# Kernel optimization log

Hardware: AMD Instinct MI355X
Metric: run time of the kernel (lower is better)

## Reference

```python
import jax, jax.numpy as jnp
import numpy as np

B, T, F, H = 64, 512, 128, 512

def _rnn(x_seq, h0, Wih, Whh, bih, bhh):
    # PyTorch vanilla RNN: h_t = tanh(x_t @ Wih^T + bih + h_{t-1} @ Whh^T + bhh)
    def step(h, x_t):
        h = jnp.tanh(x_t @ Wih.T + bih + h @ Whh.T + bhh)
        return h, h
    _, ys = jax.lax.scan(step, h0, jnp.swapaxes(x_seq, 0, 1))  # scan over time
    return jnp.swapaxes(ys, 0, 1)  # [B, T, H]

def _decode(z, Wih, Whh, bih, bhh):
    # decoder input at step t = concat(prev_output, z_t); 1-layer RNN so prev_output == h_{t-1}
    def step(h, z_t):
        u = jnp.concatenate([h, z_t], axis=-1)  # [B, 2H]
        h_new = jnp.tanh(u @ Wih.T + bih + h @ Whh.T + bhh)
        return h_new, h_new
    h0 = jnp.zeros((z.shape[0], Whh.shape[0]), z.dtype)
    _, ys = jax.lax.scan(step, h0, jnp.swapaxes(z, 0, 1))
    return jnp.swapaxes(ys, 0, 1)  # [B, T, H]

def setup_inputs() -> dict:
    key = jax.random.key(0)
    ks = jax.random.split(key, 16)
    s = 0.02
    p = {
        'x':   jax.random.normal(ks[0], (B, T, F), jnp.float32),
        'eps': jax.random.normal(ks[1], (B, T, H), jnp.float32),
        'Wih_en': jax.random.normal(ks[2], (H, F)) * s,
        'Whh_en': jax.random.normal(ks[3], (H, H)) * s,
        'bih_en': jax.random.normal(ks[4], (H,)) * s,
        'bhh_en': jax.random.normal(ks[5], (H,)) * s,
        'W_mu':  jax.random.normal(ks[6], (H, H)) * s,
        'b_mu':  jax.random.normal(ks[7], (H,)) * s,
        'W_lv':  jax.random.normal(ks[8], (H, H)) * s,
        'b_lv':  jax.random.normal(ks[9], (H,)) * s,
        'Wih_de': jax.random.normal(ks[10], (H, 2 * H)) * s,
        'Whh_de': jax.random.normal(ks[11], (H, H)) * s,
        'bih_de': jax.random.normal(ks[12], (H,)) * s,
        'bhh_de': jax.random.normal(ks[13], (H,)) * s,
        'W_mux': jax.random.normal(ks[14], (F, H)) * s,
        'b_mux': jnp.zeros((F,)),
        'W_lvx': jax.random.normal(ks[15], (F, H)) * s,
        'b_lvx': jnp.zeros((F,)),
    }
    return p

def reference(x, eps, Wih_en, Whh_en, bih_en, bhh_en, W_mu, b_mu, W_lv, b_lv,
              Wih_de, Whh_de, bih_de, bhh_de, W_mux, b_mux, W_lvx, b_lvx):
    h0 = jnp.zeros((x.shape[0], Whh_en.shape[0]), x.dtype)
    y = _rnn(x, h0, Wih_en, Whh_en, bih_en, bhh_en)                 # [B,T,H]
    mu_post = y @ W_mu.T + b_mu
    logsigma2_post = y @ W_lv.T + b_lv
    z = eps * jnp.exp(logsigma2_post / 2) + mu_post                 # reparameterize
    outputs = _decode(z, Wih_de, Whh_de, bih_de, bhh_de)            # [B,T,H]
    mu_xhat = outputs @ W_mux.T + b_mux
    logsigma2_xhat = outputs @ W_lvx.T + b_lvx
    return (mu_post, logsigma2_post, mu_xhat, logsigma2_xhat)
```

## Files before the change

kernel.cpp:

```cpp
#include <hip/hip_runtime.h>

typedef _Float16 h2_t __attribute__((ext_vector_type(2)));
typedef _Float16 h4_t __attribute__((ext_vector_type(4)));
typedef _Float16 h8_t __attribute__((ext_vector_type(8)));
typedef float    f4_t __attribute__((ext_vector_type(4)));

#define B_  64
#define T_  512
#define F_  128
#define H_  512

static __device__ __forceinline__ int d4(int acc, unsigned a, unsigned b) {
#if __has_builtin(__builtin_amdgcn_sdot4)
    return __builtin_amdgcn_sdot4((int)a, (int)b, acc, false);
#else
    #pragma unroll
    for (int i = 0; i < 4; ++i)
        acc += (int)(signed char)((a >> (8 * i)) & 0xff) *
               (int)(signed char)((b >> (8 * i)) & 0xff);
    return acc;
#endif
}
static __device__ __forceinline__ int dot16i8(int acc, uint4 w, uint4 h) {
    acc = d4(acc, w.x, h.x);
    acc = d4(acc, w.y, h.y);
    acc = d4(acc, w.z, h.z);
    acc = d4(acc, w.w, h.w);
    return acc;
}

static __device__ __forceinline__ int pair_sum(int x) {
#if __has_builtin(__builtin_amdgcn_mov_dpp)
    return x + __builtin_amdgcn_mov_dpp(x, 0xB1, 0xF, 0xF, true);
#else
    return x + __shfl_xor(x, 1);
#endif
}

__global__ void k_cast_f16(const float* __restrict__ src, _Float16* __restrict__ dst, int n) {
    int i = blockIdx.x * blockDim.x + threadIdx.x;
    if (i < n) dst[i] = (_Float16)src[i];
}

__global__ void k_prep_z(const float* __restrict__ Wih_de, _Float16* __restrict__ Wz) {
    int i = blockIdx.x * blockDim.x + threadIdx.x;
    int cc = i >> 9, kk = i & 511;
    Wz[i] = (_Float16)Wih_de[cc * 1024 + 512 + kk];
}

__global__ void k_prep_bias(const float* __restrict__ a, const float* __restrict__ b,
                            float* __restrict__ o) {
    int i = threadIdx.x;
    o[i] = a[i] + b[i];
}

__global__ void k_cat2(const float* __restrict__ a, const float* __restrict__ b,
                       float* __restrict__ o, int n) {
    int i = blockIdx.x * blockDim.x + threadIdx.x;
    if (i < 2 * n) o[i] = (i < n) ? a[i] : b[i - n];
}

__global__ void k_quant(const float* __restrict__ A, int sA,
                        const float* __restrict__ Bo, int sB,
                        signed char* __restrict__ q, float* __restrict__ fac) {
    __shared__ float red[128];
    const int c = blockIdx.x, t = threadIdx.x;
    f4_t v = *(const f4_t*)(A + (size_t)c * sA + t * 4);
    if (Bo) {
        f4_t vb = *(const f4_t*)(Bo + (size_t)c * sB + t * 4);
        v = v + vb;
    }
    float m = fmaxf(fmaxf(fabsf(v[0]), fabsf(v[1])), fmaxf(fabsf(v[2]), fabsf(v[3])));
    red[t] = m;
    __syncthreads();
    for (int o = 64; o; o >>= 1) {
        if (t < o) red[t] = fmaxf(red[t], red[t + o]);
        __syncthreads();
    }
    float mx = red[0];
    float inv = mx > 0.f ? 127.f / mx : 0.f;
    unsigned r = 0;
    #pragma unroll
    for (int i = 0; i < 4; ++i) {
        int qi = (int)rintf(fminf(fmaxf(v[i] * inv, -127.f), 127.f));
        r |= ((unsigned)(unsigned char)(signed char)qi) << (8 * i);
    }
    *(unsigned*)(q + (size_t)c * 512 + t * 4) = r;
    if (t == 0) fac[c] = mx > 0.f ? mx / 127.f : 0.f;
}

#define BM 128
#define BN 128
#define BK 32
#define LDT 40

__global__ __launch_bounds__(256) void k_gemm(
    const _Float16* __restrict__ A, const _Float16* __restrict__ Bt,
    const float* __restrict__ bias,
    float* __restrict__ Cf, float* __restrict__ Cf2, _Float16* __restrict__ Ch,
    int M, int N, int nsplit, int K) {
    __shared__ _Float16 Al[BM * LDT];
    __shared__ _Float16 Bl[BN * LDT];
    const int tid = threadIdx.x;
    const int bm = blockIdx.x * BM, bn = blockIdx.y * BN;
    const int wid = tid >> 6, lane = tid & 63;
    const int wm = (wid >> 1) * 64, wn = (wid & 1) * 64;
    const int l15 = lane & 15, l4 = lane >> 4;

    f4_t acc[4][4];
    #pragma unroll
    for (int i = 0; i < 4; ++i)
        #pragma unroll
        for (int j = 0; j < 4; ++j) {
            f4_t zz = {0.f, 0.f, 0.f, 0.f};
            acc[i][j] = zz;
        }

    const int r = tid >> 1, hf = tid & 1;
    const h8_t* gA0 = (const h8_t*)(A + (size_t)(bm + r) * K);
    const h8_t* gB0 = (const h8_t*)(Bt + (size_t)(bn + r) * K);

    for (int k0 = 0; k0 < K; k0 += BK) {
        __syncthreads();
        int kf = (k0 >> 3) + hf * 2;
        h8_t a0 = gA0[kf], a1 = gA0[kf + 1];
        h8_t b0 = gB0[kf], b1 = gB0[kf + 1];
        *(h8_t*)&Al[r * LDT + hf * 16]     = a0;
        *(h8_t*)&Al[r * LDT + hf * 16 + 8] = a1;
        *(h8_t*)&Bl[r * LDT + hf * 16]     = b0;
        *(h8_t*)&Bl[r * LDT + hf * 16 + 8] = b1;
        __syncthreads();
        h8_t af[4], bf[4];
        #pragma unroll
        for (int i = 0; i < 4; ++i) af[i] = *(const h8_t*)&Al[(wm + i * 16 + l15) * LDT + l4 * 8];
        #pragma unroll
        for (int j = 0; j < 4; ++j) bf[j] = *(const h8_t*)&Bl[(wn + j * 16 + l15) * LDT + l4 * 8];
        #pragma unroll
        for (int i = 0; i < 4; ++i)
            #pragma unroll
            for (int j = 0; j < 4; ++j)
                acc[i][j] = __builtin_amdgcn_mfma_f32_16x16x32_f16(af[i], bf[j], acc[i][j], 0, 0, 0);
    }

    const int ns2 = N - nsplit;
    #pragma unroll
    for (int i = 0; i < 4; ++i) {
        int m0 = bm + wm + i * 16 + l4 * 4;
        #pragma unroll
        for (int j = 0; j < 4; ++j) {
            int n0 = bn + wn + j * 16 + l15;
            float bb = bias ? bias[n0] : 0.f;
            #pragma unroll
            for (int rr = 0; rr < 4; ++rr) {
                float v = acc[i][j][rr] + bb;
                if (Cf) {
                    if (n0 < nsplit) Cf[(size_t)(m0 + rr) * nsplit + n0] = v;
                    else             Cf2[(size_t)(m0 + rr) * ns2 + (n0 - nsplit)] = v;
                }
                if (Ch) Ch[(size_t)(m0 + rr) * N + n0] = (_Float16)v;
            }
        }
    }
}

#define HHS 272
__global__ __launch_bounds__(512) void k_rnn(
    const signed char* __restrict__ Wq,
    const float* __restrict__ fac,
    const _Float16* __restrict__ pre,
    _Float16* __restrict__ out) {
    __shared__ __align__(16) signed char h_q[2][2 * HHS];

    const int tid = threadIdx.x;
    const int half = tid & 1;
    const int r0 = tid & ~1;
    const int r1 = tid | 1;
    const int b = blockIdx.x;

    const uint4* q0 = (const uint4*)(Wq + (size_t)r0 * 512 + half * 256);
    const uint4* q1 = (const uint4*)(Wq + (size_t)r1 * 512 + half * 256);
    uint4 wa[16], wb[16];
    #pragma unroll
    for (int j = 0; j < 16; ++j) { wa[j] = q0[j]; wb[j] = q1[j]; }
    if (tid < 34) ((uint4*)&h_q[0][0])[tid] = make_uint4(0u, 0u, 0u, 0u);
    __syncthreads();

    const size_t base = (size_t)b * T_ * H_ + tid;
    float pcur = (float)pre[base];
    const float facr = fac[tid] * (1.f / 127.f);
    const int woff = ((tid >> 8) * HHS) + (tid & 255);

    for (int t = 0; t < T_; ++t) {
        int tn = (t + 1 < T_) ? t + 1 : t;
        _Float16 pnx = pre[base + (size_t)tn * H_];

        int i0 = 0, i1 = 0;
        const uint4* hv = (const uint4*)&h_q[t & 1][half * HHS];
        #pragma unroll
        for (int j = 0; j < 16; ++j) {
            uint4 hh = hv[j];
            i0 = dot16i8(i0, wa[j], hh);
            i1 = dot16i8(i1, wb[j], hh);
        }

        int o0 = pair_sum(i0);
        int o1 = pair_sum(i1);
        int mine = half ? o1 : o0;

        float hn = tanhf((float)mine * facr + pcur);
        out[base + (size_t)t * H_] = (_Float16)hn;
        h_q[(t + 1) & 1][woff] = (signed char)(int)rintf(hn * 127.f);
        __syncthreads();
        pcur = (float)pnx;
    }
}

__global__ void k_z(const float* __restrict__ mu, const float* __restrict__ lv,
                    const float* __restrict__ eps, _Float16* __restrict__ z, int n4) {
    int i = blockIdx.x * blockDim.x + threadIdx.x;
    if (i >= n4) return;
    f4_t m = ((const f4_t*)mu)[i];
    f4_t l = ((const f4_t*)lv)[i];
    f4_t e = ((const f4_t*)eps)[i];
    h4_t r;
    #pragma unroll
    for (int j = 0; j < 4; ++j) r[j] = (_Float16)(e[j] * expf(l[j] * 0.5f) + m[j]);
    ((h4_t*)z)[i] = r;
}

extern "C" void kernel_launch(void* const* d_in, const int* in_sizes, int n_in,
                              void* d_out, int out_size, void* d_ws, size_t ws_size,
                              hipStream_t stream) {
    const float* x      = (const float*)d_in[0];
    const float* eps    = (const float*)d_in[1];
    const float* Wih_en = (const float*)d_in[2];
    const float* Whh_en = (const float*)d_in[3];
    const float* bih_en = (const float*)d_in[4];
    const float* bhh_en = (const float*)d_in[5];
    const float* W_mu   = (const float*)d_in[6];
    const float* b_mu   = (const float*)d_in[7];
    const float* W_lv   = (const float*)d_in[8];
    const float* b_lv   = (const float*)d_in[9];
    const float* Wih_de = (const float*)d_in[10];
    const float* Whh_de = (const float*)d_in[11];
    const float* bih_de = (const float*)d_in[12];
    const float* bhh_de = (const float*)d_in[13];
    const float* W_mux  = (const float*)d_in[14];
    const float* b_mux  = (const float*)d_in[15];
    const float* W_lvx  = (const float*)d_in[16];
    const float* b_lvx  = (const float*)d_in[17];
    float* out = (float*)d_out;

    char* ws = (char*)d_ws;
    _Float16* Wih_en_h = (_Float16*)(ws + 0);
    _Float16* W_mu_h   = (_Float16*)(ws + 655360);
    _Float16* W_lv_h   = (_Float16*)(ws + 1179648);
    _Float16* Wz_h     = (_Float16*)(ws + 1703936);
    _Float16* Wmux_h   = (_Float16*)(ws + 2752512);
    _Float16* Wlvx_h   = (_Float16*)(ws + 2883584);
    float*    benc     = (float*)(ws + 3014656);
    float*    bdec     = (float*)(ws + 3016704);
    signed char* Wq_en = (signed char*)(ws + 3018752);
    signed char* Wq_de = (signed char*)(ws + 3280896);
    float*    fac_en   = (float*)(ws + 3543040);
    float*    fac_de   = (float*)(ws + 3545088);
    float*    bmulv    = (float*)(ws + 3547136);
    float*    bmuxlvx  = (float*)(ws + 3551232);
    _Float16* x_h      = (_Float16*)(ws + 4194304);
    _Float16* pre_h    = (_Float16*)(ws + 12582912);
    _Float16* act_h    = (_Float16*)(ws + 46137344);
    _Float16* z_h      = (_Float16*)(ws + 79691776);

    const int thr = 256;
    k_cast_f16<<<(65536 + thr - 1) / thr, thr, 0, stream>>>(Wih_en, Wih_en_h, 65536);
    k_cast_f16<<<(262144 + thr - 1) / thr, thr, 0, stream>>>(W_mu, W_mu_h, 262144);
    k_cast_f16<<<(262144 + thr - 1) / thr, thr, 0, stream>>>(W_lv, W_lv_h, 262144);
    k_cast_f16<<<(65536 + thr - 1) / thr, thr, 0, stream>>>(W_mux, Wmux_h, 65536);
    k_cast_f16<<<(65536 + thr - 1) / thr, thr, 0, stream>>>(W_lvx, Wlvx_h, 65536);
    k_cast_f16<<<(4194304 + thr - 1) / thr, thr, 0, stream>>>(x, x_h, 4194304);
    k_prep_z<<<262144 / thr, thr, 0, stream>>>(Wih_de, Wz_h);
    k_prep_bias<<<1, 512, 0, stream>>>(bih_en, bhh_en, benc);
    k_prep_bias<<<1, 512, 0, stream>>>(bih_de, bhh_de, bdec);
    k_cat2<<<4, 256, 0, stream>>>(b_mu, b_lv, bmulv, 512);
    k_cat2<<<1, 256, 0, stream>>>(b_mux, b_lvx, bmuxlvx, 128);
    k_quant<<<512, 128, 0, stream>>>(Whh_en, 512, nullptr, 0, Wq_en, fac_en);
    k_quant<<<512, 128, 0, stream>>>(Wih_de, 1024, Whh_de, 512, Wq_de, fac_de);

    dim3 gFull(32768 / BM, 512 / BN);
    dim3 gWide(32768 / BM, 1024 / BN);
    dim3 gNarrow(32768 / BM, 256 / BN);

    k_gemm<<<gFull, 256, 0, stream>>>(x_h, Wih_en_h, benc, nullptr, nullptr, pre_h,
                                      32768, 512, 512, 128);
    k_rnn<<<64, 512, 0, stream>>>(Wq_en, fac_en, pre_h, act_h);
    k_gemm<<<gWide, 256, 0, stream>>>(act_h, W_mu_h, bmulv, out, out + 16777216, nullptr,
                                      32768, 1024, 512, 512);
    k_z<<<4194304 / thr, thr, 0, stream>>>(out, out + 16777216, eps, z_h, 4194304);
    k_gemm<<<gFull, 256, 0, stream>>>(z_h, Wz_h, bdec, nullptr, nullptr, pre_h,
                                      32768, 512, 512, 512);
    k_rnn<<<64, 512, 0, stream>>>(Wq_de, fac_de, pre_h, act_h);
    k_gemm<<<gNarrow, 256, 0, stream>>>(act_h, Wmux_h, bmuxlvx, out + 33554432, out + 37748736,
                                        nullptr, 32768, 256, 128, 512);
}
```

Measured before the change: 1.084 ms.

## Repack int8 recurrent weights coalesced and spill part of them to global reads

Adds a repack kernel that lays out the int8 recurrent weights so that consecutive threads read consecutive uint4 words. The RNN kernel now keeps only 10 of 16 weight chunks per row in registers and streams the other 6 from global memory (L2/L1) every timestep. The aim is to lower register pressure in the 512-thread recurrent kernel, avoiding spills or improving scheduling, and to make the weight loads coalesced. The cost is extra global loads inside the serial time loop, which add latency on the critical path of every step.

```diff
diff --git a/kernel.cpp b/kernel.cpp
--- a/kernel.cpp
+++ b/kernel.cpp
@@ -87,6 +87,15 @@
     }
     *(unsigned*)(q + (size_t)c * 512 + t * 4) = r;
     if (t == 0) fac[c] = mx > 0.f ? mx / 127.f : 0.f;
+}
+
+__global__ void k_repack(const signed char* __restrict__ Wq, uint4* __restrict__ W2) {
+    int gid = blockIdx.x * blockDim.x + threadIdx.x;
+    int j = gid >> 9, tid2 = gid & 511;
+    int half = tid2 & 1;
+    int row = (j < 16) ? (tid2 & ~1) : (tid2 | 1);
+    int cj = j & 15;
+    W2[gid] = *(const uint4*)(Wq + (size_t)row * 512 + half * 256 + cj * 16);
 }
 
 #define BM 128
@@ -165,7 +174,7 @@
 
 #define HHS 272
 __global__ __launch_bounds__(512) void k_rnn(
-    const signed char* __restrict__ Wq,
+    const uint4* __restrict__ W2,
     const float* __restrict__ fac,
     const _Float16* __restrict__ pre,
     _Float16* __restrict__ out) {
@@ -173,15 +182,14 @@
 
     const int tid = threadIdx.x;
     const int half = tid & 1;
-    const int r0 = tid & ~1;
-    const int r1 = tid | 1;
     const int b = blockIdx.x;
 
-    const uint4* q0 = (const uint4*)(Wq + (size_t)r0 * 512 + half * 256);
-    const uint4* q1 = (const uint4*)(Wq + (size_t)r1 * 512 + half * 256);
-    uint4 wa[16], wb[16];
-    #pragma unroll
-    for (int j = 0; j < 16; ++j) { wa[j] = q0[j]; wb[j] = q1[j]; }
+    uint4 wa[10], wb[10];
+    #pragma unroll
+    for (int j = 0; j < 10; ++j) {
+        wa[j] = W2[j * 512 + tid];
+        wb[j] = W2[(16 + j) * 512 + tid];
+    }
     if (tid < 34) ((uint4*)&h_q[0][0])[tid] = make_uint4(0u, 0u, 0u, 0u);
     __syncthreads();
 
@@ -197,10 +205,16 @@
         int i0 = 0, i1 = 0;
         const uint4* hv = (const uint4*)&h_q[t & 1][half * HHS];
         #pragma unroll
-        for (int j = 0; j < 16; ++j) {
+        for (int j = 0; j < 10; ++j) {
             uint4 hh = hv[j];
             i0 = dot16i8(i0, wa[j], hh);
             i1 = dot16i8(i1, wb[j], hh);
+        }
+        #pragma unroll
+        for (int j = 10; j < 16; ++j) {
+            uint4 hh = hv[j];
+            i0 = dot16i8(i0, W2[j * 512 + tid], hh);
+            i1 = dot16i8(i1, W2[(16 + j) * 512 + tid], hh);
         }
 
         int o0 = pair_sum(i0);
@@ -266,6 +280,8 @@
     float*    fac_de   = (float*)(ws + 3545088);
     float*    bmulv    = (float*)(ws + 3547136);
     float*    bmuxlvx  = (float*)(ws + 3551232);
+    uint4*    W2_en    = (uint4*)(ws + 3552256);
+    uint4*    W2_de    = (uint4*)(ws + 3814400);
     _Float16* x_h      = (_Float16*)(ws + 4194304);
     _Float16* pre_h    = (_Float16*)(ws + 12582912);
     _Float16* act_h    = (_Float16*)(ws + 46137344);
@@ -285,6 +301,8 @@
     k_cat2<<<1, 256, 0, stream>>>(b_mux, b_lvx, bmuxlvx, 128);
     k_quant<<<512, 128, 0, stream>>>(Whh_en, 512, nullptr, 0, Wq_en, fac_en);
     k_quant<<<512, 128, 0, stream>>>(Wih_de, 1024, Whh_de, 512, Wq_de, fac_de);
+    k_repack<<<64, 256, 0, stream>>>(Wq_en, W2_en);
+    k_repack<<<64, 256, 0, stream>>>(Wq_de, W2_de);
 
     dim3 gFull(32768 / BM, 512 / BN);
     dim3 gWide(32768 / BM, 1024 / BN);
@@ -292,13 +310,13 @@
 
     k_gemm<<<gFull, 256, 0, stream>>>(x_h, Wih_en_h, benc, nullptr, nullptr, pre_h,
                                       32768, 512, 512, 128);
-    k_rnn<<<64, 512, 0, stream>>>(Wq_en, fac_en, pre_h, act_h);
+    k_rnn<<<64, 512, 0, stream>>>(W2_en, fac_en, pre_h, act_h);
     k_gemm<<<gWide, 256, 0, stream>>>(act_h, W_mu_h, bmulv, out, out + 16777216, nullptr,
                                       32768, 1024, 512, 512);
     k_z<<<4194304 / thr, thr, 0, stream>>>(out, out + 16777216, eps, z_h, 4194304);
     k_gemm<<<gFull, 256, 0, stream>>>(z_h, Wz_h, bdec, nullptr, nullptr, pre_h,
                                       32768, 512, 512, 512);
-    k_rnn<<<64, 512, 0, stream>>>(Wq_de, fac_de, pre_h, act_h);
+    k_rnn<<<64, 512, 0, stream>>>(W2_de, fac_de, pre_h, act_h);
     k_gemm<<<gNarrow, 256, 0, stream>>>(act_h, Wmux_h, bmuxlvx, out + 33554432, out + 37748736,
                                         nullptr, 32768, 256, 128, 512);
 }
```

Result: faster. 1.045 ms (-3.6%).

## Split RNN recurrent dot products four ways with repacked int8 weights

Applied to the files above, without the earlier changes.

The recurrent kernel now has each group of four threads share four hidden rows. Each thread covers a quarter of the K dimension, and the partial sums are combined with a two-step DPP quad reduction. A new repack kernel lays the quantized weights out so each thread's slices load with coalesced uint4 reads. Three quarters of the weights stay in registers and the last quarter is re-read from global or L2 on every step. The intent is fewer LDS reads of the hidden state per step and less register pressure, at the cost of an extra reduction stage and per-step global weight loads.

```diff
diff --git a/kernel.cpp b/kernel.cpp
--- a/kernel.cpp
+++ b/kernel.cpp
@@ -29,12 +29,15 @@
     return acc;
 }
 
-static __device__ __forceinline__ int pair_sum(int x) {
+static __device__ __forceinline__ int quad_sum(int x) {
 #if __has_builtin(__builtin_amdgcn_mov_dpp)
-    return x + __builtin_amdgcn_mov_dpp(x, 0xB1, 0xF, 0xF, true);
+    x += __builtin_amdgcn_mov_dpp(x, 0xB1, 0xF, 0xF, true);
+    x += __builtin_amdgcn_mov_dpp(x, 0x4E, 0xF, 0xF, true);
 #else
-    return x + __shfl_xor(x, 1);
+    x += __shfl_xor(x, 1);
+    x += __shfl_xor(x, 2);
 #endif
+    return x;
 }
 
 __global__ void k_cast_f16(const float* __restrict__ src, _Float16* __restrict__ dst, int n) {
@@ -87,6 +90,14 @@
     }
     *(unsigned*)(q + (size_t)c * 512 + t * 4) = r;
     if (t == 0) fac[c] = mx > 0.f ? mx / 127.f : 0.f;
+}
+
+__global__ void k_repack(const signed char* __restrict__ Wq, uint4* __restrict__ W4) {
+    int gid = blockIdx.x * blockDim.x + threadIdx.x;
+    int slot = gid >> 9, tid2 = gid & 511;
+    int i = slot >> 3, j = slot & 7;
+    int q2 = tid2 & 3, g2 = tid2 >> 2;
+    W4[gid] = *(const uint4*)(Wq + (size_t)(4 * g2 + i) * 512 + q2 * 128 + j * 16);
 }
 
 #define BM 128
@@ -163,49 +174,53 @@
     }
 }
 
-#define HHS 272
+#define HQS 144
 __global__ __launch_bounds__(512) void k_rnn(
-    const signed char* __restrict__ Wq,
+    const uint4* __restrict__ W4,
     const float* __restrict__ fac,
     const _Float16* __restrict__ pre,
     _Float16* __restrict__ out) {
-    __shared__ __align__(16) signed char h_q[2][2 * HHS];
+    __shared__ __align__(16) signed char h_q[2][4 * HQS];
 
     const int tid = threadIdx.x;
-    const int half = tid & 1;
-    const int r0 = tid & ~1;
-    const int r1 = tid | 1;
+    const int q = tid & 3;
     const int b = blockIdx.x;
 
-    const uint4* q0 = (const uint4*)(Wq + (size_t)r0 * 512 + half * 256);
-    const uint4* q1 = (const uint4*)(Wq + (size_t)r1 * 512 + half * 256);
-    uint4 wa[16], wb[16];
-    #pragma unroll
-    for (int j = 0; j < 16; ++j) { wa[j] = q0[j]; wb[j] = q1[j]; }
-    if (tid < 34) ((uint4*)&h_q[0][0])[tid] = make_uint4(0u, 0u, 0u, 0u);
+    uint4 w0[8], w1[8], w2[8];
+    #pragma unroll
+    for (int j = 0; j < 8; ++j) {
+        w0[j] = W4[j * 512 + tid];
+        w1[j] = W4[(8 + j) * 512 + tid];
+        w2[j] = W4[(16 + j) * 512 + tid];
+    }
+    if (tid < 36) ((uint4*)&h_q[0][0])[tid] = make_uint4(0u, 0u, 0u, 0u);
     __syncthreads();
 
     const size_t base = (size_t)b * T_ * H_ + tid;
     float pcur = (float)pre[base];
     const float facr = fac[tid] * (1.f / 127.f);
-    const int woff = ((tid >> 8) * HHS) + (tid & 255);
+    const int woff = ((tid >> 7) * HQS) + (tid & 127);
 
     for (int t = 0; t < T_; ++t) {
         int tn = (t + 1 < T_) ? t + 1 : t;
         _Float16 pnx = pre[base + (size_t)tn * H_];
 
-        int i0 = 0, i1 = 0;
-        const uint4* hv = (const uint4*)&h_q[t & 1][half * HHS];
-        #pragma unroll
-        for (int j = 0; j < 16; ++j) {
+        int a0 = 0, a1 = 0, a2 = 0, a3 = 0;
+        const uint4* hv = (const uint4*)&h_q[t & 1][q * HQS];
+        #pragma unroll
+        for (int j = 0; j < 8; ++j) {
             uint4 hh = hv[j];
-            i0 = dot16i8(i0, wa[j], hh);
-            i1 = dot16i8(i1, wb[j], hh);
+            a0 = dot16i8(a0, w0[j], hh);
+            a1 = dot16i8(a1, w1[j], hh);
+            a2 = dot16i8(a2, w2[j], hh);
+            a3 = dot16i8(a3, W4[(24 + j) * 512 + tid], hh);
         }
 
-        int o0 = pair_sum(i0);
-        int o1 = pair_sum(i1);
-        int mine = half ? o1 : o0;
+        a0 = quad_sum(a0);
+        a1 = quad_sum(a1);
+        a2 = quad_sum(a2);
+        a3 = quad_sum(a3);
+        int mine = (q == 0) ? a0 : (q == 1) ? a1 : (q == 2) ? a2 : a3;
 
         float hn = tanhf((float)mine * facr + pcur);
         out[base + (size_t)t * H_] = (_Float16)hn;
@@ -266,6 +281,8 @@
     float*    fac_de   = (float*)(ws + 3545088);
     float*    bmulv    = (float*)(ws + 3547136);
     float*    bmuxlvx  = (float*)(ws + 3551232);
+    uint4*    W4_en    = (uint4*)(ws + 3552256);
+    uint4*    W4_de    = (uint4*)(ws + 3814400);
     _Float16* x_h      = (_Float16*)(ws + 4194304);
     _Float16* pre_h    = (_Float16*)(ws + 12582912);
     _Float16* act_h    = (_Float16*)(ws + 46137344);
@@ -285,6 +302,8 @@
     k_cat2<<<1, 256, 0, stream>>>(b_mux, b_lvx, bmuxlvx, 128);
     k_quant<<<512, 128, 0, stream>>>(Whh_en, 512, nullptr, 0, Wq_en, fac_en);
     k_quant<<<512, 128, 0, stream>>>(Wih_de, 1024, Whh_de, 512, Wq_de, fac_de);
+    k_repack<<<64, 256, 0, stream>>>(Wq_en, W4_en);
+    k_repack<<<64, 256, 0, stream>>>(Wq_de, W4_de);
 
     dim3 gFull(32768 / BM, 512 / BN);
     dim3 gWide(32768 / BM, 1024 / BN);
@@ -292,13 +311,13 @@
 
     k_gemm<<<gFull, 256, 0, stream>>>(x_h, Wih_en_h, benc, nullptr, nullptr, pre_h,
                                       32768, 512, 512, 128);
-    k_rnn<<<64, 512, 0, stream>>>(Wq_en, fac_en, pre_h, act_h);
+    k_rnn<<<64, 512, 0, stream>>>(W4_en, fac_en, pre_h, act_h);
     k_gemm<<<gWide, 256, 0, stream>>>(act_h, W_mu_h, bmulv, out, out + 16777216, nullptr,
                                       32768, 1024, 512, 512);
     k_z<<<4194304 / thr, thr, 0, stream>>>(out, out + 16777216, eps, z_h, 4194304);
     k_gemm<<<gFull, 256, 0, stream>>>(z_h, Wz_h, bdec, nullptr, nullptr, pre_h,
                                       32768, 512, 512, 512);
-    k_rnn<<<64, 512, 0, stream>>>(Wq_de, fac_de, pre_h, act_h);
+    k_rnn<<<64, 512, 0, stream>>>(W4_de, fac_de, pre_h, act_h);
     k_gemm<<<gNarrow, 256, 0, stream>>>(act_h, Wmux_h, bmuxlvx, out + 33554432, out + 37748736,
                                         nullptr, 32768, 256, 128, 512);
 }
```

After: 1.080 ms. No clear change (-0.4%).
